# Kernel optimization log

Measured on AMD Instinct MI355X. Metric: run time of the kernel, lower is better.

## Reference

```python
import jax, jax.numpy as jnp
import numpy as np

DIM = 1024
DIM_HEAD = 64
HEADS = 16
DIM_INNER = DIM_HEAD * HEADS  # 1024


def setup_inputs() -> dict:
    key = jax.random.key(0)
    k1, k2, k3 = jax.random.split(key, 3)
    b, n = 2, 2048
    x = jax.random.normal(k1, (b, n, DIM), dtype=jnp.float32)
    gamma = jnp.ones((DIM,), dtype=jnp.float32)
    # torch Linear weight [out,in] applied as x @ W.T; store pre-transposed [in,out]
    w_qkv = jax.random.normal(k2, (DIM, 3 * DIM_INNER), dtype=jnp.float32) * (DIM ** -0.5)
    w_out = jax.random.normal(k3, (DIM_INNER, DIM), dtype=jnp.float32) * (DIM_INNER ** -0.5)
    return {"x": x, "gamma": gamma, "w_qkv": w_qkv, "w_out": w_out}


def reference(x, gamma, w_qkv, w_out):
    h, d = HEADS, DIM_HEAD
    scale = d ** -0.5
    rms_scale = DIM ** 0.5
    # RMSNorm: F.normalize(x, dim=-1) * sqrt(dim) * gamma  (eps=1e-12 clamp on L2 norm)
    norm = jnp.maximum(jnp.linalg.norm(x, axis=-1, keepdims=True), 1e-12)
    xn = x / norm * rms_scale * gamma
    b, n, _ = x.shape
    qkv = xn @ w_qkv  # [b, n, 3*h*d]
    qkv = qkv.reshape(b, n, 3, h, d)
    q = qkv[:, :, 0].transpose(0, 2, 1, 3) * scale  # [b, h, n, d]
    k = qkv[:, :, 1].transpose(0, 2, 1, 3)
    v = qkv[:, :, 2].transpose(0, 2, 1, 3)
    sim = jnp.einsum('bhid,bhjd->bhij', q, k)  # [b, h, n, n]
    causal_mask = jnp.triu(jnp.ones((n, n), dtype=bool), k=1)
    neg = -jnp.finfo(sim.dtype).max
    sim = jnp.where(causal_mask, neg, sim)
    attn = jax.nn.softmax(sim, axis=-1)
    out = jnp.einsum('bhij,bhjd->bhid', attn, v)  # [b, h, n, d]
    out = out.transpose(0, 2, 1, 3).reshape(b, n, h * d)
    return out @ w_out
```

## Files before the change

### kernel.cpp

```cpp
#include <hip/hip_runtime.h>
#include <hip/hip_bf16.h>

typedef __bf16 bf16x8 __attribute__((ext_vector_type(8)));
typedef __bf16 bf16x4 __attribute__((ext_vector_type(4)));
typedef short s16x4 __attribute__((ext_vector_type(4)));
typedef float f32x4 __attribute__((ext_vector_type(4)));
typedef unsigned short u16x8 __attribute__((ext_vector_type(8)));

#define MFMA_K32(a, b, c) __builtin_amdgcn_mfma_f32_16x16x32_bf16(a, b, c, 0, 0, 0)

static __device__ __forceinline__ f32x4 mfma_k16(s16x4 a, s16x4 b, f32x4 c) {
#ifdef __HIP_DEVICE_COMPILE__
    return __builtin_amdgcn_mfma_f32_16x16x16bf16_1k(a, b, c, 0, 0, 0);
#else
    return c;
#endif
}

#define GLL16(gp, lp)                                              \
    __builtin_amdgcn_global_load_lds(                              \
        (const __attribute__((address_space(1))) void*)(gp),       \
        (__attribute__((address_space(3))) void*)(lp), 16, 0, 0)

static __device__ __forceinline__ unsigned short f2bf(float f) {
    unsigned int u = __float_as_uint(f);
    u += 0x7fffu + ((u >> 16) & 1u);
    return (unsigned short)(u >> 16);
}

__global__ __launch_bounds__(256) void transpose_cast_k(
    const float* __restrict__ in, unsigned short* __restrict__ out, int R, int C) {
    __shared__ float t[32][33];
    int c0 = blockIdx.x * 32, r0 = blockIdx.y * 32;
    int tr = threadIdx.x >> 5, tc = threadIdx.x & 31;
#pragma unroll
    for (int i = 0; i < 4; i++)
        t[tr + i * 8][tc] = in[(size_t)(r0 + tr + i * 8) * C + c0 + tc];
    __syncthreads();
#pragma unroll
    for (int i = 0; i < 4; i++)
        out[(size_t)(c0 + tr + i * 8) * R + r0 + tc] = f2bf(t[tc][tr + i * 8]);
}

__global__ __launch_bounds__(256) void rmsnorm_k(
    const float* __restrict__ x, const float* __restrict__ gamma,
    unsigned short* __restrict__ xn) {
    int row = blockIdx.x;
    int tid = threadIdx.x;
    const float* xr = x + (size_t)row * 1024;
    float4 v = *(const float4*)(xr + tid * 4);
    float ss = v.x * v.x + v.y * v.y + v.z * v.z + v.w * v.w;
#pragma unroll
    for (int off = 1; off < 64; off <<= 1) ss += __shfl_xor(ss, off, 64);
    __shared__ float red[4];
    if ((tid & 63) == 0) red[tid >> 6] = ss;
    __syncthreads();
    float tot = red[0] + red[1] + red[2] + red[3];
    float f = 32.0f / fmaxf(sqrtf(tot), 1e-12f);
    float4 g = *(const float4*)(gamma + tid * 4);
    ushort4 o;
    o.x = f2bf(v.x * f * g.x);
    o.y = f2bf(v.y * f * g.y);
    o.z = f2bf(v.z * f * g.z);
    o.w = f2bf(v.w * f * g.w);
    *(ushort4*)(xn + (size_t)row * 1024 + tid * 4) = o;
}

template <int MODE>
__global__ __launch_bounds__(256) void gemm_bt_k(
    const unsigned short* __restrict__ A, const unsigned short* __restrict__ BT,
    float* __restrict__ C, unsigned short* __restrict__ qw,
    unsigned short* __restrict__ kw, unsigned short* __restrict__ vw,
    int M, int N, int K) {
    __shared__ unsigned short As[128][32];
    __shared__ unsigned short Bs[128][32];
    int tid = threadIdx.x;
    int wave = tid >> 6, lane = tid & 63, quad = lane >> 4, l16 = lane & 15;
    int wr = wave >> 1, wc = wave & 1;
    int m0 = blockIdx.y * 128, n0 = blockIdx.x * 128;
    int lrow = lane >> 2, lcol = (lane & 3) * 8;
    const unsigned short* Ag0 = A + (size_t)(m0 + wave * 32 + lrow) * K + lcol;
    const unsigned short* Ag1 = A + (size_t)(m0 + wave * 32 + 16 + lrow) * K + lcol;
    const unsigned short* Bg0 = BT + (size_t)(n0 + wave * 32 + lrow) * K + lcol;
    const unsigned short* Bg1 = BT + (size_t)(n0 + wave * 32 + 16 + lrow) * K + lcol;
    f32x4 acc[4][4] = {};
    for (int k0 = 0; k0 < K; k0 += 32) {
        __syncthreads();
        GLL16(Ag0 + k0, &As[wave * 32][0]);
        GLL16(Ag1 + k0, &As[wave * 32 + 16][0]);
        GLL16(Bg0 + k0, &Bs[wave * 32][0]);
        GLL16(Bg1 + k0, &Bs[wave * 32 + 16][0]);
        __syncthreads();
        bf16x8 af[4], bfr[4];
#pragma unroll
        for (int t = 0; t < 4; t++) {
            af[t] = *(const bf16x8*)&As[wr * 64 + t * 16 + l16][quad * 8];
            bfr[t] = *(const bf16x8*)&Bs[wc * 64 + t * 16 + l16][quad * 8];
        }
#pragma unroll
        for (int rt = 0; rt < 4; rt++)
#pragma unroll
            for (int ct = 0; ct < 4; ct++)
                acc[rt][ct] = MFMA_K32(af[rt], bfr[ct], acc[rt][ct]);
    }
#pragma unroll
    for (int rt = 0; rt < 4; rt++) {
        int mb = m0 + wr * 64 + rt * 16 + quad * 4;
        int b = mb >> 11, nn = mb & 2047;
#pragma unroll
        for (int ct = 0; ct < 4; ct++) {
            int col = n0 + wc * 64 + ct * 16 + l16;
            if (MODE == 0) {
#pragma unroll
                for (int r = 0; r < 4; r++)
                    C[(size_t)(mb + r) * N + col] = acc[rt][ct][r];
            } else {
                int sec = col >> 10, ci = col & 1023;
                int hh = ci >> 6, dd = ci & 63;
                int bh = b * 16 + hh;
                if (sec == 0) {
#pragma unroll
                    for (int r = 0; r < 4; r++)
                        qw[((size_t)bh * 2048 + nn + r) * 64 + dd] = f2bf(acc[rt][ct][r] * 0.125f);
                } else if (sec == 1) {
#pragma unroll
                    for (int r = 0; r < 4; r++)
                        kw[((size_t)bh * 2048 + nn + r) * 64 + dd] = f2bf(acc[rt][ct][r]);
                } else {
                    ushort4 pk;
                    pk.x = f2bf(acc[rt][ct][0]);
                    pk.y = f2bf(acc[rt][ct][1]);
                    pk.z = f2bf(acc[rt][ct][2]);
                    pk.w = f2bf(acc[rt][ct][3]);
                    *(ushort4*)&vw[((size_t)bh * 64 + dd) * 2048 + nn] = pk;
                }
            }
        }
    }
}

__global__ __launch_bounds__(256) void attn_k(
    const unsigned short* __restrict__ q, const unsigned short* __restrict__ k,
    const unsigned short* __restrict__ vt, unsigned short* __restrict__ o) {
    __shared__ unsigned short Ks[64][72];
    __shared__ unsigned short Vt[64][72];
    int bh = blockIdx.y, px = blockIdx.x;
    int tid = threadIdx.x, wave = tid >> 6, lane = tid & 63;
    int quad = lane >> 4, l16 = lane & 15;
    int b = bh >> 4, h = bh & 15;
    const unsigned short* qg = q + (size_t)bh * 2048 * 64;
    const unsigned short* kg = k + (size_t)bh * 2048 * 64;
    const unsigned short* vg = vt + (size_t)bh * 64 * 2048;
    int srow = tid >> 2, scol = (tid & 3) * 16;
#pragma unroll 1
    for (int phase = 0; phase < 2; phase++) {
        int qt = phase == 0 ? (31 - px) : px;
        int q0w = qt * 64 + wave * 16;
        bf16x8 bq[2];
#pragma unroll
        for (int ks = 0; ks < 2; ks++)
            bq[ks] = *(const bf16x8*)&qg[(size_t)(q0w + l16) * 64 + ks * 32 + quad * 8];
        f32x4 ot[4] = {};
        float mrun = -1e38f, lrun = 0.f;
        int nkt = qt + 1;
        for (int kt = 0; kt < nkt; kt++) {
            __syncthreads();
            *(u16x8*)&Ks[srow][scol] = *(const u16x8*)&kg[(size_t)(kt * 64 + srow) * 64 + scol];
            *(u16x8*)&Ks[srow][scol + 8] = *(const u16x8*)&kg[(size_t)(kt * 64 + srow) * 64 + scol + 8];
            *(u16x8*)&Vt[srow][scol] = *(const u16x8*)&vg[(size_t)srow * 2048 + kt * 64 + scol];
            *(u16x8*)&Vt[srow][scol + 8] = *(const u16x8*)&vg[(size_t)srow * 2048 + kt * 64 + scol + 8];
            __syncthreads();
            f32x4 sf[4];
#pragma unroll
            for (int ct = 0; ct < 4; ct++) {
                bf16x8 ak0 = *(const bf16x8*)&Ks[ct * 16 + l16][quad * 8];
                bf16x8 ak1 = *(const bf16x8*)&Ks[ct * 16 + l16][32 + quad * 8];
                f32x4 s = {};
                s = MFMA_K32(ak0, bq[0], s);
                s = MFMA_K32(ak1, bq[1], s);
                sf[ct] = s;
            }
            if (kt == qt) {
                int qloc = wave * 16 + l16;
#pragma unroll
                for (int ct = 0; ct < 4; ct++)
#pragma unroll
                    for (int r = 0; r < 4; r++)
                        if (ct * 16 + quad * 4 + r > qloc) sf[ct][r] = -1e30f;
            }
            float mx = -1e30f;
#pragma unroll
            for (int ct = 0; ct < 4; ct++)
#pragma unroll
                for (int r = 0; r < 4; r++) mx = fmaxf(mx, sf[ct][r]);
            mx = fmaxf(mx, __shfl_xor(mx, 16, 64));
            mx = fmaxf(mx, __shfl_xor(mx, 32, 64));
            float mnew = fmaxf(mrun, mx);
            float al = __expf(mrun - mnew);
            mrun = mnew;
            float rs = 0.f;
#pragma unroll
            for (int ct = 0; ct < 4; ct++)
#pragma unroll
                for (int r = 0; r < 4; r++) {
                    float p = __expf(sf[ct][r] - mnew);
                    sf[ct][r] = p;
                    rs += p;
                }
            rs += __shfl_xor(rs, 16, 64);
            rs += __shfl_xor(rs, 32, 64);
            lrun = lrun * al + rs;
            s16x4 bpr[4];
#pragma unroll
            for (int ct = 0; ct < 4; ct++) {
#pragma unroll
                for (int r = 0; r < 4; r++) bpr[ct][r] = (short)f2bf(sf[ct][r]);
            }
#pragma unroll
            for (int dt = 0; dt < 4; dt++) {
#pragma unroll
                for (int r = 0; r < 4; r++) ot[dt][r] *= al;
#pragma unroll
                for (int ct = 0; ct < 4; ct++) {
                    s16x4 av = *(const s16x4*)&Vt[dt * 16 + l16][ct * 16 + quad * 4];
                    ot[dt] = mfma_k16(av, bpr[ct], ot[dt]);
                }
            }
        }
        float inv = 1.0f / lrun;
        size_t rowbase = ((size_t)b * 2048 + q0w + l16) * 1024 + h * 64;
#pragma unroll
        for (int dt = 0; dt < 4; dt++) {
            ushort4 pk;
            pk.x = f2bf(ot[dt][0] * inv);
            pk.y = f2bf(ot[dt][1] * inv);
            pk.z = f2bf(ot[dt][2] * inv);
            pk.w = f2bf(ot[dt][3] * inv);
            *(ushort4*)&o[rowbase + dt * 16 + quad * 4] = pk;
        }
    }
}

extern "C" void kernel_launch(void* const* d_in, const int* in_sizes, int n_in,
                              void* d_out, int out_size, void* d_ws, size_t ws_size,
                              hipStream_t stream) {
    const float* x = (const float*)d_in[0];
    const float* gamma = (const float*)d_in[1];
    const float* w_qkv = (const float*)d_in[2];
    const float* w_out = (const float*)d_in[3];
    float* out = (float*)d_out;
    char* ws = (char*)d_ws;

    unsigned short* xn = (unsigned short*)(ws);
    unsigned short* wtq = (unsigned short*)(ws + 8388608);
    unsigned short* wto = (unsigned short*)(ws + 14680064);
    unsigned short* qw = (unsigned short*)(ws + 16777216);
    unsigned short* kw = (unsigned short*)(ws + 25165824);
    unsigned short* vw = (unsigned short*)(ws + 33554432);
    unsigned short* ao = xn;

    transpose_cast_k<<<dim3(96, 32), 256, 0, stream>>>(w_qkv, wtq, 1024, 3072);
    transpose_cast_k<<<dim3(32, 32), 256, 0, stream>>>(w_out, wto, 1024, 1024);
    rmsnorm_k<<<4096, 256, 0, stream>>>(x, gamma, xn);
    gemm_bt_k<1><<<dim3(24, 32), 256, 0, stream>>>(xn, wtq, nullptr, qw, kw, vw,
                                                   4096, 3072, 1024);
    attn_k<<<dim3(16, 32), 256, 0, stream>>>(qw, kw, vw, ao);
    gemm_bt_k<0><<<dim3(8, 32), 256, 0, stream>>>(ao, wto, out, nullptr, nullptr, nullptr,
                                                  4096, 1024, 1024);
}
```

Baseline: 214.8 us.

## Fuse prep kernels, double-buffer attention K/V, use exp2 and packed bf16 converts

Merges the two weight transpose-casts and the RMSNorm into one launch. Attention now double-buffers the K/V tiles in LDS, loading the next tile into registers while the current one is computed, and drops one barrier per iteration. The log2(e) factor is folded into the Q scale so softmax can use the hardware exp2 builtin. Packed bf16 conversion instructions replace the scalar rounding code. The output projection GEMM gets a 64-row tile variant so it launches more blocks. LDS use in attention doubles, and the packed convert's rounding may differ slightly from the manual round-to-nearest-even.

```diff
diff --git a/kernel.cpp b/kernel.cpp
--- a/kernel.cpp
+++ b/kernel.cpp
@@ -2,7 +2,6 @@
 #include <hip/hip_bf16.h>
 
 typedef __bf16 bf16x8 __attribute__((ext_vector_type(8)));
-typedef __bf16 bf16x4 __attribute__((ext_vector_type(4)));
 typedef short s16x4 __attribute__((ext_vector_type(4)));
 typedef float f32x4 __attribute__((ext_vector_type(4)));
 typedef unsigned short u16x8 __attribute__((ext_vector_type(8)));
@@ -17,6 +16,14 @@
 #endif
 }
 
+static __device__ __forceinline__ float fast_exp2(float x) {
+#ifdef __HIP_DEVICE_COMPILE__
+    return __builtin_amdgcn_exp2f(x);
+#else
+    return x;
+#endif
+}
+
 #define GLL16(gp, lp)                                              \
     __builtin_amdgcn_global_load_lds(                              \
         (const __attribute__((address_space(1))) void*)(gp),       \
@@ -28,88 +35,117 @@
     return (unsigned short)(u >> 16);
 }
 
-__global__ __launch_bounds__(256) void transpose_cast_k(
-    const float* __restrict__ in, unsigned short* __restrict__ out, int R, int C) {
-    __shared__ float t[32][33];
-    int c0 = blockIdx.x * 32, r0 = blockIdx.y * 32;
-    int tr = threadIdx.x >> 5, tc = threadIdx.x & 31;
-#pragma unroll
-    for (int i = 0; i < 4; i++)
-        t[tr + i * 8][tc] = in[(size_t)(r0 + tr + i * 8) * C + c0 + tc];
-    __syncthreads();
-#pragma unroll
-    for (int i = 0; i < 4; i++)
-        out[(size_t)(c0 + tr + i * 8) * R + r0 + tc] = f2bf(t[tc][tr + i * 8]);
-}
-
-__global__ __launch_bounds__(256) void rmsnorm_k(
+static __device__ __forceinline__ unsigned int cvtpk_bf16(float lo, float hi) {
+#if defined(__HIP_DEVICE_COMPILE__) && __has_builtin(__builtin_amdgcn_cvt_pk_bf16_f32)
+    typedef __bf16 bf16x2 __attribute__((ext_vector_type(2)));
+    bf16x2 r = __builtin_amdgcn_cvt_pk_bf16_f32(lo, hi);
+    return __builtin_bit_cast(unsigned int, r);
+#else
+    return (unsigned int)f2bf(lo) | ((unsigned int)f2bf(hi) << 16);
+#endif
+}
+
+#define LOG2E 1.44269504088896340736f
+
+__global__ __launch_bounds__(256) void prep_k(
     const float* __restrict__ x, const float* __restrict__ gamma,
-    unsigned short* __restrict__ xn) {
-    int row = blockIdx.x;
-    int tid = threadIdx.x;
-    const float* xr = x + (size_t)row * 1024;
-    float4 v = *(const float4*)(xr + tid * 4);
-    float ss = v.x * v.x + v.y * v.y + v.z * v.z + v.w * v.w;
-#pragma unroll
-    for (int off = 1; off < 64; off <<= 1) ss += __shfl_xor(ss, off, 64);
-    __shared__ float red[4];
-    if ((tid & 63) == 0) red[tid >> 6] = ss;
-    __syncthreads();
-    float tot = red[0] + red[1] + red[2] + red[3];
-    float f = 32.0f / fmaxf(sqrtf(tot), 1e-12f);
-    float4 g = *(const float4*)(gamma + tid * 4);
-    ushort4 o;
-    o.x = f2bf(v.x * f * g.x);
-    o.y = f2bf(v.y * f * g.y);
-    o.z = f2bf(v.z * f * g.z);
-    o.w = f2bf(v.w * f * g.w);
-    *(ushort4*)(xn + (size_t)row * 1024 + tid * 4) = o;
-}
-
-template <int MODE>
+    const float* __restrict__ w_qkv, const float* __restrict__ w_out,
+    unsigned short* __restrict__ xn, unsigned short* __restrict__ wtq,
+    unsigned short* __restrict__ wto) {
+    __shared__ float sm[32][33];
+    int bid = blockIdx.x, tid = threadIdx.x;
+    if (bid < 4096) {
+        const float* in;
+        unsigned short* out;
+        int R = 1024, C, bx, by;
+        if (bid < 3072) { in = w_qkv; out = wtq; C = 3072; bx = bid % 96; by = bid / 96; }
+        else { int b2 = bid - 3072; in = w_out; out = wto; C = 1024; bx = b2 % 32; by = b2 / 32; }
+        int c0 = bx * 32, r0 = by * 32;
+        int tr = tid >> 5, tc = tid & 31;
+#pragma unroll
+        for (int i = 0; i < 4; i++)
+            sm[tr + i * 8][tc] = in[(size_t)(r0 + tr + i * 8) * C + c0 + tc];
+        __syncthreads();
+#pragma unroll
+        for (int i = 0; i < 4; i++)
+            out[(size_t)(c0 + tr + i * 8) * R + r0 + tc] = f2bf(sm[tc][tr + i * 8]);
+    } else {
+        int row = bid - 4096;
+        const float* xr = x + (size_t)row * 1024;
+        float4 v = *(const float4*)(xr + tid * 4);
+        float ss = v.x * v.x + v.y * v.y + v.z * v.z + v.w * v.w;
+#pragma unroll
+        for (int off = 1; off < 64; off <<= 1) ss += __shfl_xor(ss, off, 64);
+        if ((tid & 63) == 0) sm[0][tid >> 6] = ss;
+        __syncthreads();
+        float tot = sm[0][0] + sm[0][1] + sm[0][2] + sm[0][3];
+        float f = 32.0f / fmaxf(sqrtf(tot), 1e-12f);
+        float4 g = *(const float4*)(gamma + tid * 4);
+        uint2 o;
+        o.x = cvtpk_bf16(v.x * f * g.x, v.y * f * g.y);
+        o.y = cvtpk_bf16(v.z * f * g.z, v.w * f * g.w);
+        *(uint2*)(xn + (size_t)row * 1024 + tid * 4) = o;
+    }
+}
+
+template <int MODE, int BM>
 __global__ __launch_bounds__(256) void gemm_bt_k(
     const unsigned short* __restrict__ A, const unsigned short* __restrict__ BT,
     float* __restrict__ C, unsigned short* __restrict__ qw,
     unsigned short* __restrict__ kw, unsigned short* __restrict__ vw,
     int M, int N, int K) {
-    __shared__ unsigned short As[128][32];
+    constexpr int RT = 4;
+    constexpr int CT = (BM == 128) ? 4 : 2;
+    __shared__ unsigned short As[BM][32];
     __shared__ unsigned short Bs[128][32];
     int tid = threadIdx.x;
     int wave = tid >> 6, lane = tid & 63, quad = lane >> 4, l16 = lane & 15;
-    int wr = wave >> 1, wc = wave & 1;
-    int m0 = blockIdx.y * 128, n0 = blockIdx.x * 128;
+    int wrb, wcb;
+    if constexpr (BM == 128) { wrb = (wave >> 1) * 64; wcb = (wave & 1) * 64; }
+    else { wrb = 0; wcb = wave * 32; }
+    int m0 = blockIdx.y * BM, n0 = blockIdx.x * 128;
     int lrow = lane >> 2, lcol = (lane & 3) * 8;
-    const unsigned short* Ag0 = A + (size_t)(m0 + wave * 32 + lrow) * K + lcol;
-    const unsigned short* Ag1 = A + (size_t)(m0 + wave * 32 + 16 + lrow) * K + lcol;
+    const unsigned short *Ag0, *Ag1 = nullptr;
+    if constexpr (BM == 128) {
+        Ag0 = A + (size_t)(m0 + wave * 32 + lrow) * K + lcol;
+        Ag1 = A + (size_t)(m0 + wave * 32 + 16 + lrow) * K + lcol;
+    } else {
+        Ag0 = A + (size_t)(m0 + wave * 16 + lrow) * K + lcol;
+    }
     const unsigned short* Bg0 = BT + (size_t)(n0 + wave * 32 + lrow) * K + lcol;
     const unsigned short* Bg1 = BT + (size_t)(n0 + wave * 32 + 16 + lrow) * K + lcol;
-    f32x4 acc[4][4] = {};
+    f32x4 acc[RT][CT] = {};
     for (int k0 = 0; k0 < K; k0 += 32) {
         __syncthreads();
-        GLL16(Ag0 + k0, &As[wave * 32][0]);
-        GLL16(Ag1 + k0, &As[wave * 32 + 16][0]);
+        if constexpr (BM == 128) {
+            GLL16(Ag0 + k0, &As[wave * 32][0]);
+            GLL16(Ag1 + k0, &As[wave * 32 + 16][0]);
+        } else {
+            GLL16(Ag0 + k0, &As[wave * 16][0]);
+        }
         GLL16(Bg0 + k0, &Bs[wave * 32][0]);
         GLL16(Bg1 + k0, &Bs[wave * 32 + 16][0]);
         __syncthreads();
-        bf16x8 af[4], bfr[4];
-#pragma unroll
-        for (int t = 0; t < 4; t++) {
-            af[t] = *(const bf16x8*)&As[wr * 64 + t * 16 + l16][quad * 8];
-            bfr[t] = *(const bf16x8*)&Bs[wc * 64 + t * 16 + l16][quad * 8];
-        }
-#pragma unroll
-        for (int rt = 0; rt < 4; rt++)
-#pragma unroll
-            for (int ct = 0; ct < 4; ct++)
+        bf16x8 af[RT], bfr[CT];
+#pragma unroll
+        for (int t = 0; t < RT; t++)
+            af[t] = *(const bf16x8*)&As[wrb + t * 16 + l16][quad * 8];
+#pragma unroll
+        for (int t = 0; t < CT; t++)
+            bfr[t] = *(const bf16x8*)&Bs[wcb + t * 16 + l16][quad * 8];
+#pragma unroll
+        for (int rt = 0; rt < RT; rt++)
+#pragma unroll
+            for (int ct = 0; ct < CT; ct++)
                 acc[rt][ct] = MFMA_K32(af[rt], bfr[ct], acc[rt][ct]);
     }
 #pragma unroll
-    for (int rt = 0; rt < 4; rt++) {
-        int mb = m0 + wr * 64 + rt * 16 + quad * 4;
+    for (int rt = 0; rt < RT; rt++) {
+        int mb = m0 + wrb + rt * 16 + quad * 4;
         int b = mb >> 11, nn = mb & 2047;
 #pragma unroll
-        for (int ct = 0; ct < 4; ct++) {
-            int col = n0 + wc * 64 + ct * 16 + l16;
+        for (int ct = 0; ct < CT; ct++) {
+            int col = n0 + wcb + ct * 16 + l16;
             if (MODE == 0) {
 #pragma unroll
                 for (int r = 0; r < 4; r++)
@@ -121,18 +157,17 @@
                 if (sec == 0) {
 #pragma unroll
                     for (int r = 0; r < 4; r++)
-                        qw[((size_t)bh * 2048 + nn + r) * 64 + dd] = f2bf(acc[rt][ct][r] * 0.125f);
+                        qw[((size_t)bh * 2048 + nn + r) * 64 + dd] =
+                            f2bf(acc[rt][ct][r] * (0.125f * LOG2E));
                 } else if (sec == 1) {
 #pragma unroll
                     for (int r = 0; r < 4; r++)
                         kw[((size_t)bh * 2048 + nn + r) * 64 + dd] = f2bf(acc[rt][ct][r]);
                 } else {
-                    ushort4 pk;
-                    pk.x = f2bf(acc[rt][ct][0]);
-                    pk.y = f2bf(acc[rt][ct][1]);
-                    pk.z = f2bf(acc[rt][ct][2]);
-                    pk.w = f2bf(acc[rt][ct][3]);
-                    *(ushort4*)&vw[((size_t)bh * 64 + dd) * 2048 + nn] = pk;
+                    uint2 pk;
+                    pk.x = cvtpk_bf16(acc[rt][ct][0], acc[rt][ct][1]);
+                    pk.y = cvtpk_bf16(acc[rt][ct][2], acc[rt][ct][3]);
+                    *(uint2*)&vw[((size_t)bh * 64 + dd) * 2048 + nn] = pk;
                 }
             }
         }
@@ -142,8 +177,8 @@
 __global__ __launch_bounds__(256) void attn_k(
     const unsigned short* __restrict__ q, const unsigned short* __restrict__ k,
     const unsigned short* __restrict__ vt, unsigned short* __restrict__ o) {
-    __shared__ unsigned short Ks[64][72];
-    __shared__ unsigned short Vt[64][72];
+    __shared__ unsigned short Ks[2][64][72];
+    __shared__ unsigned short Vt[2][64][72];
     int bh = blockIdx.y, px = blockIdx.x;
     int tid = threadIdx.x, wave = tid >> 6, lane = tid & 63;
     int quad = lane >> 4, l16 = lane & 15;
@@ -152,6 +187,7 @@
     const unsigned short* kg = k + (size_t)bh * 2048 * 64;
     const unsigned short* vg = vt + (size_t)bh * 64 * 2048;
     int srow = tid >> 2, scol = (tid & 3) * 16;
+    u16x8 pk0, pk1, pv0, pv1;
 #pragma unroll 1
     for (int phase = 0; phase < 2; phase++) {
         int qt = phase == 0 ? (31 - px) : px;
@@ -163,18 +199,35 @@
         f32x4 ot[4] = {};
         float mrun = -1e38f, lrun = 0.f;
         int nkt = qt + 1;
+        {
+            const unsigned short* kp = kg + (size_t)srow * 64 + scol;
+            pk0 = *(const u16x8*)kp;
+            pk1 = *(const u16x8*)(kp + 8);
+            const unsigned short* vp = vg + (size_t)srow * 2048 + scol;
+            pv0 = *(const u16x8*)vp;
+            pv1 = *(const u16x8*)(vp + 8);
+            *(u16x8*)&Ks[0][srow][scol] = pk0;
+            *(u16x8*)&Ks[0][srow][scol + 8] = pk1;
+            *(u16x8*)&Vt[0][srow][scol] = pv0;
+            *(u16x8*)&Vt[0][srow][scol + 8] = pv1;
+        }
+        __syncthreads();
         for (int kt = 0; kt < nkt; kt++) {
-            __syncthreads();
-            *(u16x8*)&Ks[srow][scol] = *(const u16x8*)&kg[(size_t)(kt * 64 + srow) * 64 + scol];
-            *(u16x8*)&Ks[srow][scol + 8] = *(const u16x8*)&kg[(size_t)(kt * 64 + srow) * 64 + scol + 8];
-            *(u16x8*)&Vt[srow][scol] = *(const u16x8*)&vg[(size_t)srow * 2048 + kt * 64 + scol];
-            *(u16x8*)&Vt[srow][scol + 8] = *(const u16x8*)&vg[(size_t)srow * 2048 + kt * 64 + scol + 8];
-            __syncthreads();
+            int cb = kt & 1;
+            bool pf = (kt + 1 < nkt);
+            if (pf) {
+                const unsigned short* kp = kg + (size_t)((kt + 1) * 64 + srow) * 64 + scol;
+                pk0 = *(const u16x8*)kp;
+                pk1 = *(const u16x8*)(kp + 8);
+                const unsigned short* vp = vg + (size_t)srow * 2048 + (kt + 1) * 64 + scol;
+                pv0 = *(const u16x8*)vp;
+                pv1 = *(const u16x8*)(vp + 8);
+            }
             f32x4 sf[4];
 #pragma unroll
             for (int ct = 0; ct < 4; ct++) {
-                bf16x8 ak0 = *(const bf16x8*)&Ks[ct * 16 + l16][quad * 8];
-                bf16x8 ak1 = *(const bf16x8*)&Ks[ct * 16 + l16][32 + quad * 8];
+                bf16x8 ak0 = *(const bf16x8*)&Ks[cb][ct * 16 + l16][quad * 8];
+                bf16x8 ak1 = *(const bf16x8*)&Ks[cb][ct * 16 + l16][32 + quad * 8];
                 f32x4 s = {};
                 s = MFMA_K32(ak0, bq[0], s);
                 s = MFMA_K32(ak1, bq[1], s);
@@ -196,14 +249,14 @@
             mx = fmaxf(mx, __shfl_xor(mx, 16, 64));
             mx = fmaxf(mx, __shfl_xor(mx, 32, 64));
             float mnew = fmaxf(mrun, mx);
-            float al = __expf(mrun - mnew);
+            float al = fast_exp2(mrun - mnew);
             mrun = mnew;
             float rs = 0.f;
 #pragma unroll
             for (int ct = 0; ct < 4; ct++)
 #pragma unroll
                 for (int r = 0; r < 4; r++) {
-                    float p = __expf(sf[ct][r] - mnew);
+                    float p = fast_exp2(sf[ct][r] - mnew);
                     sf[ct][r] = p;
                     rs += p;
                 }
@@ -213,8 +266,10 @@
             s16x4 bpr[4];
 #pragma unroll
             for (int ct = 0; ct < 4; ct++) {
-#pragma unroll
-                for (int r = 0; r < 4; r++) bpr[ct][r] = (short)f2bf(sf[ct][r]);
+                uint2 u;
+                u.x = cvtpk_bf16(sf[ct][0], sf[ct][1]);
+                u.y = cvtpk_bf16(sf[ct][2], sf[ct][3]);
+                bpr[ct] = __builtin_bit_cast(s16x4, u);
             }
 #pragma unroll
             for (int dt = 0; dt < 4; dt++) {
@@ -222,21 +277,26 @@
                 for (int r = 0; r < 4; r++) ot[dt][r] *= al;
 #pragma unroll
                 for (int ct = 0; ct < 4; ct++) {
-                    s16x4 av = *(const s16x4*)&Vt[dt * 16 + l16][ct * 16 + quad * 4];
+                    s16x4 av = *(const s16x4*)&Vt[cb][dt * 16 + l16][ct * 16 + quad * 4];
                     ot[dt] = mfma_k16(av, bpr[ct], ot[dt]);
                 }
             }
+            if (pf) {
+                *(u16x8*)&Ks[1 - cb][srow][scol] = pk0;
+                *(u16x8*)&Ks[1 - cb][srow][scol + 8] = pk1;
+                *(u16x8*)&Vt[1 - cb][srow][scol] = pv0;
+                *(u16x8*)&Vt[1 - cb][srow][scol + 8] = pv1;
+            }
+            __syncthreads();
         }
         float inv = 1.0f / lrun;
         size_t rowbase = ((size_t)b * 2048 + q0w + l16) * 1024 + h * 64;
 #pragma unroll
         for (int dt = 0; dt < 4; dt++) {
-            ushort4 pk;
-            pk.x = f2bf(ot[dt][0] * inv);
-            pk.y = f2bf(ot[dt][1] * inv);
-            pk.z = f2bf(ot[dt][2] * inv);
-            pk.w = f2bf(ot[dt][3] * inv);
-            *(ushort4*)&o[rowbase + dt * 16 + quad * 4] = pk;
+            uint2 pk;
+            pk.x = cvtpk_bf16(ot[dt][0] * inv, ot[dt][1] * inv);
+            pk.y = cvtpk_bf16(ot[dt][2] * inv, ot[dt][3] * inv);
+            *(uint2*)&o[rowbase + dt * 16 + quad * 4] = pk;
         }
     }
 }
@@ -259,12 +319,10 @@
     unsigned short* vw = (unsigned short*)(ws + 33554432);
     unsigned short* ao = xn;
 
-    transpose_cast_k<<<dim3(96, 32), 256, 0, stream>>>(w_qkv, wtq, 1024, 3072);
-    transpose_cast_k<<<dim3(32, 32), 256, 0, stream>>>(w_out, wto, 1024, 1024);
-    rmsnorm_k<<<4096, 256, 0, stream>>>(x, gamma, xn);
-    gemm_bt_k<1><<<dim3(24, 32), 256, 0, stream>>>(xn, wtq, nullptr, qw, kw, vw,
-                                                   4096, 3072, 1024);
+    prep_k<<<8192, 256, 0, stream>>>(x, gamma, w_qkv, w_out, xn, wtq, wto);
+    gemm_bt_k<1, 128><<<dim3(24, 32), 256, 0, stream>>>(xn, wtq, nullptr, qw, kw, vw,
+                                                        4096, 3072, 1024);
     attn_k<<<dim3(16, 32), 256, 0, stream>>>(qw, kw, vw, ao);
-    gemm_bt_k<0><<<dim3(8, 32), 256, 0, stream>>>(ao, wto, out, nullptr, nullptr, nullptr,
-                                                  4096, 1024, 1024);
-}
+    gemm_bt_k<0, 64><<<dim3(8, 64), 256, 0, stream>>>(ao, wto, out, nullptr, nullptr,
+                                                      nullptr, 4096, 1024, 1024);
+}
```

Measured after the change: 195.4 us. -9.0%, faster.
